# Kernel optimization log

Hardware: AMD Instinct MI355X
Metric: run time of the kernel (lower is better)

The kernel has to match this reference:

```python
import jax, jax.numpy as jnp
import numpy as np

N0, N1, N2 = 80000, 40000, 20000
E1, E2 = 500000, 250000
FIN = 128        # in_channels
H = 2            # heads
C1 = 64          # hidden_channels -> layer1 out per head (concat -> 128)
C2 = 64          # out_channels -> layer2 out per head (mean over heads)
ED = 10          # edge_dim per embedding, total edge feat = 2*ED = 20
NTYPE, NTS = 23, 1158


def setup_inputs() -> dict:
    key = jax.random.key(0)
    ks = jax.random.split(key, 48)
    sc = 0.05
    inp = {
        "x": jax.random.normal(ks[0], (N0, FIN), jnp.float32),
        "ei1_src": jax.random.randint(ks[1], (E1,), 0, N0),
        "ei1_dst": jax.random.randint(ks[2], (E1,), 0, N1),
        "et1": jax.random.randint(ks[3], (E1,), 0, NTYPE),
        "ets1": jax.random.randint(ks[4], (E1,), 0, NTS),
        "ei2_src": jax.random.randint(ks[5], (E2,), 0, N1),
        "ei2_dst": jax.random.randint(ks[6], (E2,), 0, N2),
        "et2": jax.random.randint(ks[7], (E2,), 0, NTYPE),
        "ets2": jax.random.randint(ks[8], (E2,), 0, NTS),
        # shared edge embeddings (Linear(23,10), Linear(1158,10))
        "edge_W": jax.random.normal(ks[9], (ED, NTYPE), jnp.float32) * sc,
        "edge_b": jax.random.normal(ks[10], (ED,), jnp.float32) * sc,
        "time_W": jax.random.normal(ks[11], (ED, NTS), jnp.float32) * sc,
        "time_b": jax.random.normal(ks[12], (ED,), jnp.float32) * sc,
    }
    # layer 1: in=128, heads=2, C=64, concat=True (out dim 128)
    hc1 = H * C1
    inp["Wq1"] = jax.random.normal(ks[13], (hc1, FIN), jnp.float32) * sc
    inp["bq1"] = jnp.zeros((hc1,), jnp.float32)
    inp["Wk1"] = jax.random.normal(ks[14], (hc1, FIN), jnp.float32) * sc
    inp["bk1"] = jnp.zeros((hc1,), jnp.float32)
    inp["Wv1"] = jax.random.normal(ks[15], (hc1, FIN), jnp.float32) * sc
    inp["bv1"] = jnp.zeros((hc1,), jnp.float32)
    inp["We1"] = jax.random.normal(ks[16], (hc1, 2 * ED), jnp.float32) * sc
    inp["Wskip1"] = jax.random.normal(ks[17], (hc1, FIN), jnp.float32) * sc
    inp["bskip1"] = jnp.zeros((hc1,), jnp.float32)
    inp["Wbeta1"] = jax.random.normal(ks[18], (1, 3 * hc1), jnp.float32) * sc
    inp["ln_g"] = jnp.ones((hc1,), jnp.float32)
    inp["ln_b"] = jnp.zeros((hc1,), jnp.float32)
    # layer 2: in=128, heads=2, C=64, concat=False (out dim 64)
    hc2 = H * C2
    inp["Wq2"] = jax.random.normal(ks[19], (hc2, hc1), jnp.float32) * sc
    inp["bq2"] = jnp.zeros((hc2,), jnp.float32)
    inp["Wk2"] = jax.random.normal(ks[20], (hc2, hc1), jnp.float32) * sc
    inp["bk2"] = jnp.zeros((hc2,), jnp.float32)
    inp["Wv2"] = jax.random.normal(ks[21], (hc2, hc1), jnp.float32) * sc
    inp["bv2"] = jnp.zeros((hc2,), jnp.float32)
    inp["We2"] = jax.random.normal(ks[22], (hc2, 2 * ED), jnp.float32) * sc
    inp["Wskip2"] = jax.random.normal(ks[23], (C2, hc1), jnp.float32) * sc
    inp["bskip2"] = jnp.zeros((C2,), jnp.float32)
    inp["Wbeta2"] = jax.random.normal(ks[24], (1, 3 * C2), jnp.float32) * sc
    return inp


def _edge_feat(et, ets, edge_W, edge_b, time_W, time_b):
    # one_hot(e) @ W.T + b == W.T[e] + b (avoids materializing huge one-hot)
    return jnp.concatenate([jnp.take(edge_W.T, et, axis=0) + edge_b,
                            jnp.take(time_W.T, ets, axis=0) + time_b], axis=-1)


def _conv(x_src, x_dst, src, dst, ef, Wq, bq, Wk, bk, Wv, bv, We,
          Wskip, bskip, Wbeta, concat):
    n_dst = x_dst.shape[0]
    HC = Wq.shape[0]
    C = HC // H
    q = (x_dst @ Wq.T + bq).reshape(n_dst, H, C)            # [Nd,H,C]
    k = (x_src @ Wk.T + bk)[src].reshape(-1, H, C)          # [E,H,C]
    v = (x_src @ Wv.T + bv)[src].reshape(-1, H, C)
    e = (ef @ We.T).reshape(-1, H, C)
    k = k + e
    alpha = jnp.einsum('ehc,ehc->eh', q[dst], k) / np.sqrt(C).astype(np.float32)
    # segment softmax over destination nodes
    m = jax.ops.segment_max(alpha, dst, num_segments=n_dst)
    ex = jnp.exp(alpha - m[dst])
    s = jax.ops.segment_sum(ex, dst, num_segments=n_dst)
    a = ex / (s[dst] + 1e-16)                               # [E,H]
    msg = (v + e) * a[..., None]                            # [E,H,C]
    out = jax.ops.segment_sum(msg.reshape(-1, HC), dst, num_segments=n_dst)
    out = out if concat else out.reshape(n_dst, H, C).mean(axis=1)
    x_r = x_dst @ Wskip.T + bskip
    beta = jax.nn.sigmoid(
        jnp.concatenate([out, x_r, out - x_r], axis=-1) @ Wbeta.T)  # [Nd,1]
    return beta * x_r + (1.0 - beta) * out


def _layernorm(x, g, b):
    mu = x.mean(-1, keepdims=True)
    var = x.var(-1, keepdims=True)
    return (x - mu) / jnp.sqrt(var + 1e-5) * g + b


def reference(x, ei1_src, ei1_dst, et1, ets1, ei2_src, ei2_dst, et2, ets2,
              edge_W, edge_b, time_W, time_b,
              Wq1, bq1, Wk1, bk1, Wv1, bv1, We1, Wskip1, bskip1, Wbeta1,
              ln_g, ln_b,
              Wq2, bq2, Wk2, bk2, Wv2, bv2, We2, Wskip2, bskip2, Wbeta2):
    ef1 = _edge_feat(et1, ets1, edge_W, edge_b, time_W, time_b)
    h = _conv(x, x[:N1], ei1_src, ei1_dst, ef1,
              Wq1, bq1, Wk1, bk1, Wv1, bv1, We1, Wskip1, bskip1, Wbeta1,
              concat=True)
    h = jax.nn.gelu(_layernorm(h, ln_g, ln_b), approximate=False)
    ef2 = _edge_feat(et2, ets2, edge_W, edge_b, time_W, time_b)
    o = _conv(h, h[:N2], ei2_src, ei2_dst, ef2,
              Wq2, bq2, Wk2, bk2, Wv2, bv2, We2, Wskip2, bskip2, Wbeta2,
              concat=False)
    return jax.nn.log_softmax(o, axis=-1)
```

## Files before the change

### kernel.cpp

```cpp
#include <hip/hip_runtime.h>
#include <math.h>

#define N0 80000
#define N1 40000
#define N2 20000
#define E1C 500000
#define E2C 250000
#define NTYPE 23
#define NTS 1158

#define NB1 157
#define NB2 79
#define KV1B 1250
#define QR1B 625
#define CNTB 2930
#define KV2B 625
#define QR2B 313
#define FILLB 2930

#define OFF_XB    0u
#define OFF_QR1   5120000u
#define OFF_KV1   15360000u
#define OFF_H     25600000u
#define OFF_QR2   28160000u
#define OFF_KV2   32000000u
#define OFF_WB1   37120000u
#define OFF_BP1   37160000u
#define OFF_WB2   37170000u
#define OFF_BP2   37200000u
#define OFF_TA1   37210000u
#define OFF_TB1   37213000u
#define OFF_TA2   37370000u
#define OFF_TB2   37373000u
#define OFF_RP1   37530000u
#define OFF_CUR1  37580000u
#define OFF_ED1   37630000u
#define OFF_BS1   38640000u
#define OFF_RP2   38650000u
#define OFF_CUR2  38680000u
#define OFF_ED2   38710000u
#define OFF_BS2   39220000u
#define OFF_DONE  39230000u
#define OFF_RK1   39240000u
#define OFF_RK2   39740000u

typedef __bf16 bf16x8 __attribute__((ext_vector_type(8)));
typedef float f32x4 __attribute__((ext_vector_type(4)));

static __device__ __forceinline__ float b2f(unsigned short u) {
    union { unsigned int i; float f; } c;
    c.i = ((unsigned int)u) << 16;
    return c.f;
}
static __device__ __forceinline__ unsigned short f2b(float f) {
    unsigned int u = __float_as_uint(f);
    unsigned int r = (u + 0x7fffu + ((u >> 16) & 1u)) >> 16;
    return (unsigned short)r;
}
static __device__ __forceinline__ bf16x8 ldfrag(const unsigned short* p) {
    return *reinterpret_cast<const bf16x8*>(p);
}

static __device__ __forceinline__ void stage16(const void* g, void* l) {
    __builtin_amdgcn_global_load_lds(
        (const __attribute__((address_space(1))) unsigned int*)g,
        (__attribute__((address_space(3))) unsigned int*)l,
        16, 0, 0);
}

template <int CTRL>
static __device__ __forceinline__ float dpp_addstep(float v) {
    int x = __builtin_amdgcn_mov_dpp(__float_as_int(v), CTRL, 0xF, 0xF, true);
    return v + __int_as_float(x);
}
static __device__ __forceinline__ float red16(float v) {
    v = dpp_addstep<0xB1>(v);
    v = dpp_addstep<0x4E>(v);
    v = dpp_addstep<0x141>(v);
    v = dpp_addstep<0x140>(v);
    return v;
}
template <int CTRL>
static __device__ __forceinline__ float dpp_maxstep(float v) {
    int x = __builtin_amdgcn_mov_dpp(__float_as_int(v), CTRL, 0xF, 0xF, true);
    return fmaxf(v, __int_as_float(x));
}
static __device__ __forceinline__ float red16max(float v) {
    v = dpp_maxstep<0xB1>(v);
    v = dpp_maxstep<0x4E>(v);
    v = dpp_maxstep<0x141>(v);
    v = dpp_maxstep<0x140>(v);
    return v;
}

#define LDSS 136
#define SMEM_USHORTS 16384

template <int NTILES>
static __device__ __forceinline__ void dev_gemm_bf16out(
    const unsigned short* __restrict__ XB, const unsigned short* __restrict__ WB,
    const float* __restrict__ BP, unsigned short* __restrict__ Y, int n, int blk,
    unsigned short* sb) {
    constexpr int COLS = NTILES * 16;
    constexpr int HALF = NTILES / 2;
    constexpr int HCOLS = HALF * 16;
    constexpr int NCHUNK = (NTILES + 3) / 4;
    int wave = threadIdx.x >> 6, lane = threadIdx.x & 63;
    int m = lane & 15, quad = lane >> 4;
    int rowbase = blk * 64 + wave * 16;
    int arow = rowbase + m; if (arow >= n) arow = n - 1;
    unsigned short* swave = sb + wave * 16 * LDSS;
    const unsigned short* xrow = XB + (size_t)arow * 128 + quad * 8;
    bf16x8 a0 = ldfrag(xrow), a1 = ldfrag(xrow + 32);
    bf16x8 a2 = ldfrag(xrow + 64), a3 = ldfrag(xrow + 96);
    f32x4 acc[NTILES];
#pragma unroll
    for (int t = 0; t < NTILES; t++) acc[t] = (f32x4){0.f, 0.f, 0.f, 0.f};
    const char* gstage = (const char*)WB + wave * 1024 + lane * 16;
#pragma unroll
    for (int i = 0; i < 4; i++)
        stage16(gstage + (size_t)i * 4096, (char*)sb + wave * 1024 + i * 4096);
    __syncthreads();
#pragma unroll
    for (int c = 0; c < NCHUNK; c++) {
        if (c + 1 < NCHUNK) {
            char* lbase = (char*)sb + ((c + 1) & 1) * 16384 + wave * 1024;
#pragma unroll
            for (int i = 0; i < 4; i++)
                if ((c + 1) * 4 + i < NTILES)
                    stage16(gstage + (size_t)((c + 1) * 4 + i) * 4096,
                            lbase + i * 4096);
        }
        const unsigned short* cbase = sb + (c & 1) * 8192;
#pragma unroll
        for (int t = 0; t < 4; t++) {
            int tt = c * 4 + t;
            if (tt < NTILES) {
                const unsigned short* wt = cbase + t * 2048 + lane * 8;
                acc[tt] = __builtin_amdgcn_mfma_f32_16x16x32_bf16(a0, ldfrag(wt), acc[tt], 0, 0, 0);
                acc[tt] = __builtin_amdgcn_mfma_f32_16x16x32_bf16(a1, ldfrag(wt + 512), acc[tt], 0, 0, 0);
                acc[tt] = __builtin_amdgcn_mfma_f32_16x16x32_bf16(a2, ldfrag(wt + 1024), acc[tt], 0, 0, 0);
                acc[tt] = __builtin_amdgcn_mfma_f32_16x16x32_bf16(a3, ldfrag(wt + 1536), acc[tt], 0, 0, 0);
            }
        }
        __syncthreads();
    }
    int tswz_bit = (quad >> 1) & 1;
#pragma unroll
    for (int half = 0; half < 2; half++) {
#pragma unroll
        for (int t = 0; t < HALF; t++) {
            int tt = half * HALF + t;
            int tsw = t ^ tswz_bit;
            float b = BP[tt * 16 + m];
#pragma unroll
            for (int r = 0; r < 4; r++)
                swave[(quad * 4 + r) * LDSS + tsw * 16 + m] = f2b(acc[tt][r] + b);
        }
#pragma unroll
        for (int i = 0; i < 4; i++) {
            int idx = i * 64 + lane;
            int r = idx / (HCOLS / 8), g = idx % (HCOLS / 8);
            int gs = g ^ (((r >> 3) & 1) << 1);
            int grow = rowbase + r;
            if (grow < n) {
                uint4 v = *(const uint4*)&swave[r * LDSS + gs * 8];
                *(uint4*)(Y + (size_t)grow * COLS + half * HCOLS + g * 8) = v;
            }
        }
    }
}

template <int NTILES>
static __device__ __forceinline__ void dev_gemm_f32out(
    const unsigned short* __restrict__ XB, const unsigned short* __restrict__ WB,
    const float* __restrict__ BP, float* __restrict__ Y, int n, int blk,
    unsigned short* sb) {
    constexpr int COLS = NTILES * 16;
    constexpr int NCHUNK = (NTILES + 3) / 4;
    int wave = threadIdx.x >> 6, lane = threadIdx.x & 63;
    int m = lane & 15, quad = lane >> 4;
    int rowbase = blk * 64 + wave * 16;
    int arow = rowbase + m; if (arow >= n) arow = n - 1;
    const unsigned short* xrow = XB + (size_t)arow * 128 + quad * 8;
    bf16x8 a0 = ldfrag(xrow), a1 = ldfrag(xrow + 32);
    bf16x8 a2 = ldfrag(xrow + 64), a3 = ldfrag(xrow + 96);
    f32x4 acc[NTILES];
#pragma unroll
    for (int t = 0; t < NTILES; t++) acc[t] = (f32x4){0.f, 0.f, 0.f, 0.f};
    const char* gstage = (const char*)WB + wave * 1024 + lane * 16;
#pragma unroll
    for (int i = 0; i < 4; i++)
        stage16(gstage + (size_t)i * 4096, (char*)sb + wave * 1024 + i * 4096);
    __syncthreads();
#pragma unroll
    for (int c = 0; c < NCHUNK; c++) {
        if (c + 1 < NCHUNK) {
            char* lbase = (char*)sb + ((c + 1) & 1) * 16384 + wave * 1024;
#pragma unroll
            for (int i = 0; i < 4; i++)
                if ((c + 1) * 4 + i < NTILES)
                    stage16(gstage + (size_t)((c + 1) * 4 + i) * 4096,
                            lbase + i * 4096);
        }
        const unsigned short* cbase = sb + (c & 1) * 8192;
#pragma unroll
        for (int t = 0; t < 4; t++) {
            int tt = c * 4 + t;
            if (tt < NTILES) {
                const unsigned short* wt = cbase + t * 2048 + lane * 8;
                acc[tt] = __builtin_amdgcn_mfma_f32_16x16x32_bf16(a0, ldfrag(wt), acc[tt], 0, 0, 0);
                acc[tt] = __builtin_amdgcn_mfma_f32_16x16x32_bf16(a1, ldfrag(wt + 512), acc[tt], 0, 0, 0);
                acc[tt] = __builtin_amdgcn_mfma_f32_16x16x32_bf16(a2, ldfrag(wt + 1024), acc[tt], 0, 0, 0);
                acc[tt] = __builtin_amdgcn_mfma_f32_16x16x32_bf16(a3, ldfrag(wt + 1536), acc[tt], 0, 0, 0);
            }
        }
        __syncthreads();
    }
#pragma unroll
    for (int t = 0; t < NTILES; t++) {
        float b = BP[t * 16 + m];
#pragma unroll
        for (int r = 0; r < 4; r++) {
            int grow = rowbase + quad * 4 + r;
            if (grow < n) Y[(size_t)grow * COLS + t * 16 + m] = acc[t][r] + b;
        }
    }
}

__global__ __launch_bounds__(256) void prep(
    const float* __restrict__ x, unsigned short* __restrict__ XB,
    const float* __restrict__ Wk1, const float* __restrict__ Wv1,
    const float* __restrict__ Wq1, const float* __restrict__ Wskip1,
    const float* __restrict__ bk1, const float* __restrict__ bv1,
    const float* __restrict__ bq1, const float* __restrict__ bskip1,
    const float* __restrict__ Wk2, const float* __restrict__ Wv2,
    const float* __restrict__ Wq2, const float* __restrict__ Wskip2,
    const float* __restrict__ bk2, const float* __restrict__ bv2,
    const float* __restrict__ bq2, const float* __restrict__ bskip2,
    unsigned short* __restrict__ WB1, float* __restrict__ BP1,
    unsigned short* __restrict__ WB2, float* __restrict__ BP2,
    const float* __restrict__ edge_W, const float* __restrict__ edge_b,
    const float* __restrict__ time_W, const float* __restrict__ time_b,
    const float* __restrict__ We1, const float* __restrict__ We2,
    float* __restrict__ TA1, float* __restrict__ TB1,
    float* __restrict__ TA2, float* __restrict__ TB2,
    int* __restrict__ cnt1, int* __restrict__ cnt2, int* __restrict__ done) {
    int tid = blockIdx.x * blockDim.x + threadIdx.x;
    int stride = gridDim.x * blockDim.x;
    for (int i = tid; i < N0 * 32; i += stride) {
        float4 v = *(const float4*)(x + (size_t)i * 4);
        ushort4 u;
        u.x = f2b(v.x); u.y = f2b(v.y); u.z = f2b(v.z); u.w = f2b(v.w);
        *(ushort4*)(XB + (size_t)i * 4) = u;
    }
    for (int i = tid; i < 512 * 128; i += stride) {
        int j = i & 7, l = (i >> 3) & 63, ks = (i >> 9) & 3, t = i >> 11;
        int row = t * 16 + (l & 15);
        int col = ks * 32 + ((l >> 4) & 3) * 8 + j;
        const float* w; int off;
        if (row < 128) { w = Wk1; off = 0; }
        else if (row < 256) { w = Wv1; off = 128; }
        else if (row < 384) { w = Wq1; off = 256; }
        else { w = Wskip1; off = 384; }
        WB1[i] = f2b(w[(size_t)(row - off) * 128 + col]);
    }
    for (int i = tid; i < 512; i += stride) {
        const float* b; int off;
        if (i < 128) { b = bk1; off = 0; }
        else if (i < 256) { b = bv1; off = 128; }
        else if (i < 384) { b = bq1; off = 256; }
        else { b = bskip1; off = 384; }
        BP1[i] = b[i - off];
    }
    for (int i = tid; i < 448 * 128; i += stride) {
        int j = i & 7, l = (i >> 3) & 63, ks = (i >> 9) & 3, t = i >> 11;
        int row = t * 16 + (l & 15);
        int col = ks * 32 + ((l >> 4) & 3) * 8 + j;
        const float* w; int off;
        if (row < 128) { w = Wk2; off = 0; }
        else if (row < 256) { w = Wv2; off = 128; }
        else if (row < 384) { w = Wq2; off = 256; }
        else { w = Wskip2; off = 384; }
        WB2[i] = f2b(w[(size_t)(row - off) * 128 + col]);
    }
    for (int i = tid; i < 448; i += stride) {
        const float* b; int off;
        if (i < 128) { b = bk2; off = 0; }
        else if (i < 256) { b = bv2; off = 128; }
        else if (i < 384) { b = bq2; off = 256; }
        else { b = bskip2; off = 384; }
        BP2[i] = b[i - off];
    }
    const int TBL = (NTYPE + NTS) * 128;
    for (int i = tid; i < TBL; i += stride) {
        if (i < NTYPE * 128) {
            int e = i >> 7, c = i & 127;
            float s1 = 0.f, s2 = 0.f;
#pragma unroll
            for (int j = 0; j < 10; j++) {
                float fj = edge_W[j * NTYPE + e] + edge_b[j];
                s1 += fj * We1[c * 20 + j];
                s2 += fj * We2[c * 20 + j];
            }
            TA1[i] = s1; TA2[i] = s2;
        } else {
            int u = i - NTYPE * 128;
            int ts = u >> 7, c = u & 127;
            float s1 = 0.f, s2 = 0.f;
#pragma unroll
            for (int j = 0; j < 10; j++) {
                float fj = time_W[j * NTS + ts] + time_b[j];
                s1 += fj * We1[c * 20 + 10 + j];
                s2 += fj * We2[c * 20 + 10 + j];
            }
            TB1[u] = s1; TB2[u] = s2;
        }
    }
    for (int i = tid; i < N1 + N2 + 2; i += stride) {
        if (i < N1) cnt1[i] = 0;
        else if (i < N1 + N2) cnt2[i - N1] = 0;
        else done[i - N1 - N2] = 0;
    }
}

__global__ __launch_bounds__(256) void mega_l1(
    const unsigned short* __restrict__ XB,
    const unsigned short* __restrict__ WB1, const float* __restrict__ BP1,
    unsigned short* __restrict__ KV1, float* __restrict__ QR1,
    const int* __restrict__ d1, const int* __restrict__ d2,
    int* __restrict__ cnt1, int* __restrict__ cnt2,
    int* __restrict__ rk1, int* __restrict__ rk2) {
    __shared__ __align__(16) unsigned short sbuf[SMEM_USHORTS];
    int b = blockIdx.x;
    if (b < CNTB) {
        int t = b * 256 + threadIdx.x;
        if (t < E1C) rk1[t] = atomicAdd(&cnt1[d1[t]], 1);
        else {
            t -= E1C;
            if (t < E2C) rk2[t] = atomicAdd(&cnt2[d2[t]], 1);
        }
    } else if (b < CNTB + KV1B) {
        dev_gemm_bf16out<16>(XB, WB1, BP1, KV1, N0, b - CNTB, sbuf);
    } else {
        dev_gemm_f32out<16>(XB, WB1 + 256 * 128, BP1 + 256, QR1, N1,
                            b - CNTB - KV1B, sbuf);
    }
}

__global__ __launch_bounds__(256) void gemm_l2(
    const unsigned short* __restrict__ H,
    const unsigned short* __restrict__ WB2, const float* __restrict__ BP2,
    unsigned short* __restrict__ KV2, float* __restrict__ QR2) {
    __shared__ __align__(16) unsigned short sbuf[SMEM_USHORTS];
    int b = blockIdx.x;
    if (b < KV2B) dev_gemm_bf16out<16>(H, WB2, BP2, KV2, N1, b, sbuf);
    else dev_gemm_f32out<12>(H, WB2 + 256 * 128, BP2 + 256, QR2, N2, b - KV2B, sbuf);
}

__global__ __launch_bounds__(256) void csr_scan(
    int* __restrict__ cnt1, int* __restrict__ bs1, int* __restrict__ rp1,
    int* __restrict__ cnt2, int* __restrict__ bs2, int* __restrict__ rp2,
    int* __restrict__ done) {
    __shared__ int s[256];
    __shared__ int amlast;
    int b = blockIdx.x;
    int* cnt; int* bs; int* rp; int n, lb;
    if (b < NB1) { cnt = cnt1; bs = bs1; rp = rp1; n = N1; lb = b; }
    else { cnt = cnt2; bs = bs2; rp = rp2; n = N2; lb = b - NB1; }
    int t = lb * 256 + threadIdx.x;
    int v = (t < n) ? cnt[t] : 0;
    s[threadIdx.x] = v;
    __syncthreads();
    for (int off = 128; off; off >>= 1) {
        if (threadIdx.x < off) s[threadIdx.x] += s[threadIdx.x + off];
        __syncthreads();
    }
    if (threadIdx.x == 0) {
        atomicExch(&bs[lb], s[0]);
        __threadfence();
        int prev = atomicAdd(&done[0], 1);
        amlast = (prev == NB1 + NB2 - 1) ? 1 : 0;
    }
    __syncthreads();
    if (amlast) {
        int tt = threadIdx.x;
        int v1 = (tt < NB1) ? atomicAdd(&bs1[tt], 0) : 0;
        s[tt] = v1;
        __syncthreads();
        for (int off = 1; off < 256; off <<= 1) {
            int u = (tt >= off) ? s[tt - off] : 0;
            __syncthreads();
            s[tt] += u;
            __syncthreads();
        }
        if (tt < NB1) atomicExch(&bs1[tt], s[tt] - v1);
        __syncthreads();
        int v2 = (tt < NB2) ? atomicAdd(&bs2[tt], 0) : 0;
        s[tt] = v2;
        __syncthreads();
        for (int off = 1; off < 256; off <<= 1) {
            int u = (tt >= off) ? s[tt - off] : 0;
            __syncthreads();
            s[tt] += u;
            __syncthreads();
        }
        if (tt < NB2) atomicExch(&bs2[tt], s[tt] - v2);
        __threadfence();
        __syncthreads();
        if (tt == 0) atomicExch(&done[1], 1);
    }
    if (threadIdx.x == 0) {
        while (atomicAdd(&done[1], 0) == 0) __builtin_amdgcn_s_sleep(1);
    }
    __syncthreads();
    __threadfence();
    int base = atomicAdd(&bs[lb], 0);
    s[threadIdx.x] = v;
    __syncthreads();
    for (int off = 1; off < 256; off <<= 1) {
        int u = (threadIdx.x >= off) ? s[threadIdx.x - off] : 0;
        __syncthreads();
        s[threadIdx.x] += u;
        __syncthreads();
    }
    int incl = s[threadIdx.x];
    if (t < n) rp[t] = base + incl - v;
    if (t == n - 1) rp[n] = base + incl;
}

__global__ __launch_bounds__(256) void fill_both(
    const int* __restrict__ d1, const int* __restrict__ s1,
    const int* __restrict__ et1, const int* __restrict__ ets1,
    const int* __restrict__ rp1, const int* __restrict__ rk1, uint2* __restrict__ ed1,
    const int* __restrict__ d2, const int* __restrict__ s2,
    const int* __restrict__ et2, const int* __restrict__ ets2,
    const int* __restrict__ rp2, const int* __restrict__ rk2, uint2* __restrict__ ed2) {
    int t = blockIdx.x * 256 + threadIdx.x;
    if (t < E1C) {
        int pos = rp1[d1[t]] + rk1[t];
        ed1[pos] = make_uint2((unsigned)s1[t],
                              (unsigned)(et1[t] | (ets1[t] << 16)));
    } else {
        t -= E1C;
        if (t < E2C) {
            int pos = rp2[d2[t]] + rk2[t];
            ed2[pos] = make_uint2((unsigned)s2[t],
                                  (unsigned)(et2[t] | (ets2[t] << 16)));
        }
    }
}

static __device__ __forceinline__ void edge_accum(
    int beg, int end, int s, int co, float4 q4,
    const uint2* __restrict__ ED, const float* __restrict__ TA,
    const float* __restrict__ TB, const unsigned short* __restrict__ KV,
    float& ax, float& ay, float& az, float& aw, float& suma) {
    int p = beg + s;
    if (p >= end) return;

    uint2 dA, dB, dC;
    float4 taA, tbA, taB, tbB, taC, tbC;
    ushort4 kuA, vuA, kuB, vuB, kuC, vuC;

    dA = ED[p];
    int pA = p + 2; bool mA = pA < end;
    dB = ED[mA ? pA : beg];
    int pB = p + 4; bool mB = pB < end;
    dC = ED[mB ? pB : beg];

#define LOADSET(SET, DSC) { \
    int sn_ = (int)DSC.x, t_ = (int)(DSC.y & 0xFFFF), ts_ = (int)(DSC.y >> 16); \
    ta##SET = *(const float4*)(TA + t_ * 128 + co); \
    tb##SET = *(const float4*)(TB + ts_ * 128 + co); \
    const unsigned short* kv_ = KV + (size_t)sn_ * 256; \
    ku##SET = *(const ushort4*)(kv_ + co); \
    vu##SET = *(const ushort4*)(kv_ + 128 + co); }

#define COMPUTE(SET) { \
    float e0c = ta##SET.x + tb##SET.x, e1c = ta##SET.y + tb##SET.y; \
    float e2c = ta##SET.z + tb##SET.z, e3c = ta##SET.w + tb##SET.w; \
    float pp = q4.x * (b2f(ku##SET.x) + e0c) + q4.y * (b2f(ku##SET.y) + e1c) \
             + q4.z * (b2f(ku##SET.z) + e2c) + q4.w * (b2f(ku##SET.w) + e3c); \
    pp = red16(pp); \
    float a = __expf(pp * 0.125f); \
    ax += a * (b2f(vu##SET.x) + e0c); ay += a * (b2f(vu##SET.y) + e1c); \
    az += a * (b2f(vu##SET.z) + e2c); aw += a * (b2f(vu##SET.w) + e3c); \
    suma += a; }

    LOADSET(A, dA)
    LOADSET(B, dB)
    for (;;) {
        {
            int pC = pB + 2; bool mC = pC < end;
            dA = ED[mC ? pC : beg];
            LOADSET(C, dC)
            COMPUTE(A)
            if (!mA) break;
            mA = mB; mB = mC; pB = pC;
        }
        {
            int pC = pB + 2; bool mC = pC < end;
            dB = ED[mC ? pC : beg];
            LOADSET(A, dA)
            COMPUTE(B)
            if (!mA) break;
            mA = mB; mB = mC; pB = pC;
        }
        {
            int pC = pB + 2; bool mC = pC < end;
            dC = ED[mC ? pC : beg];
            LOADSET(B, dB)
            COMPUTE(C)
            if (!mA) break;
            mA = mB; mB = mC; pB = pC;
        }
    }
#undef LOADSET
#undef COMPUTE
}

__global__ __launch_bounds__(256) void agg_layer1(
    const int* __restrict__ rowptr, const uint2* __restrict__ ED,
    const float* __restrict__ TA, const float* __restrict__ TB,
    const float* __restrict__ QR, const unsigned short* __restrict__ KV,
    const float* __restrict__ Wbeta,
    const float* __restrict__ ln_g, const float* __restrict__ ln_b,
    unsigned short* __restrict__ hout, int n) {
    int wid = (blockIdx.x * blockDim.x + threadIdx.x) >> 6;
    int lane = threadIdx.x & 63;
    if (wid >= n) return;
    int s = lane >> 5, cg = lane & 15;
    int co = ((lane >> 4) & 1) * 64 + 4 * cg;
    int beg = rowptr[wid], end = rowptr[wid + 1];
    float4 q4 = *(const float4*)(QR + (size_t)wid * 256 + co);
    float ax = 0.f, ay = 0.f, az = 0.f, aw = 0.f, suma = 0.f;
    edge_accum(beg, end, s, co, q4, ED, TA, TB, KV, ax, ay, az, aw, suma);
    ax += __shfl_xor(ax, 32); ay += __shfl_xor(ay, 32);
    az += __shfl_xor(az, 32); aw += __shfl_xor(aw, 32);
    suma += __shfl_xor(suma, 32);
    float inv_s = 1.f / (suma + 1e-16f);
    float ox = ax * inv_s, oy = ay * inv_s, oz = az * inv_s, ow = aw * inv_s;
    float4 r4 = *(const float4*)(QR + (size_t)wid * 256 + 128 + co);
    float4 wo = *(const float4*)(Wbeta + co);
    float4 wr = *(const float4*)(Wbeta + 128 + co);
    float4 wd = *(const float4*)(Wbeta + 256 + co);
    float pb = wo.x * ox + wr.x * r4.x + wd.x * (ox - r4.x)
             + wo.y * oy + wr.y * r4.y + wd.y * (oy - r4.y)
             + wo.z * oz + wr.z * r4.z + wd.z * (oz - r4.z)
             + wo.w * ow + wr.w * r4.w + wd.w * (ow - r4.w);
    pb = red16(pb);
    pb += __shfl_xor(pb, 16);
    float beta = 1.f / (1.f + __expf(-pb));
    float gx = beta * r4.x + (1.f - beta) * ox;
    float gy = beta * r4.y + (1.f - beta) * oy;
    float gz = beta * r4.z + (1.f - beta) * oz;
    float gw = beta * r4.w + (1.f - beta) * ow;
    float sm = gx + gy + gz + gw;
    float sq = gx * gx + gy * gy + gz * gz + gw * gw;
    sm = red16(sm); sm += __shfl_xor(sm, 16);
    sq = red16(sq); sq += __shfl_xor(sq, 16);
    float mu = sm * (1.f / 128.f);
    float var = sq * (1.f / 128.f) - mu * mu;
    float inv = rsqrtf(var + 1e-5f);
    float4 lg = *(const float4*)(ln_g + co);
    float4 lb = *(const float4*)(ln_b + co);
    float yx = (gx - mu) * inv * lg.x + lb.x;
    float yy = (gy - mu) * inv * lg.y + lb.y;
    float yz = (gz - mu) * inv * lg.z + lb.z;
    float yw = (gw - mu) * inv * lg.w + lb.w;
    const float ISQ2 = 0.70710678118654752f;
    yx = 0.5f * yx * (1.f + erff(yx * ISQ2));
    yy = 0.5f * yy * (1.f + erff(yy * ISQ2));
    yz = 0.5f * yz * (1.f + erff(yz * ISQ2));
    yw = 0.5f * yw * (1.f + erff(yw * ISQ2));
    if (s == 0) {
        ushort4 hv;
        hv.x = f2b(yx); hv.y = f2b(yy); hv.z = f2b(yz); hv.w = f2b(yw);
        *(ushort4*)(hout + (size_t)wid * 128 + co) = hv;
    }
}

__global__ __launch_bounds__(256) void agg_layer2(
    const int* __restrict__ rowptr, const uint2* __restrict__ ED,
    const float* __restrict__ TA, const float* __restrict__ TB,
    const float* __restrict__ QR, const unsigned short* __restrict__ KV,
    const float* __restrict__ Wbeta,
    float* __restrict__ o, int n) {
    int wid = (blockIdx.x * blockDim.x + threadIdx.x) >> 6;
    int lane = threadIdx.x & 63;
    if (wid >= n) return;
    int s = lane >> 5, cg = lane & 15;
    int co = ((lane >> 4) & 1) * 64 + 4 * cg;
    int beg = rowptr[wid], end = rowptr[wid + 1];
    float4 q4 = *(const float4*)(QR + (size_t)wid * 192 + co);
    float ax = 0.f, ay = 0.f, az = 0.f, aw = 0.f, suma = 0.f;
    edge_accum(beg, end, s, co, q4, ED, TA, TB, KV, ax, ay, az, aw, suma);
    ax += __shfl_xor(ax, 32); ay += __shfl_xor(ay, 32);
    az += __shfl_xor(az, 32); aw += __shfl_xor(aw, 32);
    suma += __shfl_xor(suma, 32);
    float inv_s = 1.f / (suma + 1e-16f);
    float ox = ax * inv_s, oy = ay * inv_s, oz = az * inv_s, ow = aw * inv_s;
    ox = 0.5f * (ox + __shfl_xor(ox, 16));
    oy = 0.5f * (oy + __shfl_xor(oy, 16));
    oz = 0.5f * (oz + __shfl_xor(oz, 16));
    ow = 0.5f * (ow + __shfl_xor(ow, 16));
    float4 r4 = *(const float4*)(QR + (size_t)wid * 192 + 128 + 4 * cg);
    float4 wo = *(const float4*)(Wbeta + 4 * cg);
    float4 wr = *(const float4*)(Wbeta + 64 + 4 * cg);
    float4 wd = *(const float4*)(Wbeta + 128 + 4 * cg);
    float pb = wo.x * ox + wr.x * r4.x + wd.x * (ox - r4.x)
             + wo.y * oy + wr.y * r4.y + wd.y * (oy - r4.y)
             + wo.z * oz + wr.z * r4.z + wd.z * (oz - r4.z)
             + wo.w * ow + wr.w * r4.w + wd.w * (ow - r4.w);
    pb = red16(pb);
    float beta = 1.f / (1.f + __expf(-pb));
    float vx = beta * r4.x + (1.f - beta) * ox;
    float vy = beta * r4.y + (1.f - beta) * oy;
    float vz = beta * r4.z + (1.f - beta) * oz;
    float vw = beta * r4.w + (1.f - beta) * ow;
    float m = fmaxf(fmaxf(vx, vy), fmaxf(vz, vw));
    m = red16max(m);
    float se = __expf(vx - m) + __expf(vy - m) + __expf(vz - m) + __expf(vw - m);
    se = red16(se);
    float lse = m + logf(se);
    if (lane < 16)
        *(float4*)(o + (size_t)wid * 64 + 4 * cg) =
            make_float4(vx - lse, vy - lse, vz - lse, vw - lse);
}

extern "C" void kernel_launch(void* const* d_in, const int* in_sizes, int n_in,
                              void* d_out, int out_size, void* d_ws, size_t ws_size,
                              hipStream_t stream) {
    const float* x        = (const float*)d_in[0];
    const int*   ei1_src  = (const int*)d_in[1];
    const int*   ei1_dst  = (const int*)d_in[2];
    const int*   et1      = (const int*)d_in[3];
    const int*   ets1     = (const int*)d_in[4];
    const int*   ei2_src  = (const int*)d_in[5];
    const int*   ei2_dst  = (const int*)d_in[6];
    const int*   et2      = (const int*)d_in[7];
    const int*   ets2     = (const int*)d_in[8];
    const float* edge_W   = (const float*)d_in[9];
    const float* edge_b   = (const float*)d_in[10];
    const float* time_W   = (const float*)d_in[11];
    const float* time_b   = (const float*)d_in[12];
    const float* Wq1      = (const float*)d_in[13];
    const float* bq1      = (const float*)d_in[14];
    const float* Wk1      = (const float*)d_in[15];
    const float* bk1      = (const float*)d_in[16];
    const float* Wv1      = (const float*)d_in[17];
    const float* bv1      = (const float*)d_in[18];
    const float* We1      = (const float*)d_in[19];
    const float* Wskip1   = (const float*)d_in[20];
    const float* bskip1   = (const float*)d_in[21];
    const float* Wbeta1   = (const float*)d_in[22];
    const float* ln_g     = (const float*)d_in[23];
    const float* ln_b     = (const float*)d_in[24];
    const float* Wq2      = (const float*)d_in[25];
    const float* bq2      = (const float*)d_in[26];
    const float* Wk2      = (const float*)d_in[27];
    const float* bk2      = (const float*)d_in[28];
    const float* Wv2      = (const float*)d_in[29];
    const float* bv2      = (const float*)d_in[30];
    const float* We2      = (const float*)d_in[31];
    const float* Wskip2   = (const float*)d_in[32];
    const float* bskip2   = (const float*)d_in[33];
    const float* Wbeta2   = (const float*)d_in[34];

    float* ws = (float*)d_ws;
    unsigned short* xb  = (unsigned short*)(ws + OFF_XB);
    float* qr1          = ws + OFF_QR1;
    unsigned short* kv1 = (unsigned short*)(ws + OFF_KV1);
    unsigned short* h   = (unsigned short*)(ws + OFF_H);
    float* qr2          = ws + OFF_QR2;
    unsigned short* kv2 = (unsigned short*)(ws + OFF_KV2);
    unsigned short* wb1 = (unsigned short*)(ws + OFF_WB1);
    float* bp1          = ws + OFF_BP1;
    unsigned short* wb2 = (unsigned short*)(ws + OFF_WB2);
    float* bp2          = ws + OFF_BP2;
    float* ta1          = ws + OFF_TA1;
    float* tb1          = ws + OFF_TB1;
    float* ta2          = ws + OFF_TA2;
    float* tb2          = ws + OFF_TB2;
    int*   rp1          = (int*)(ws + OFF_RP1);
    int*   cur1         = (int*)(ws + OFF_CUR1);
    uint2* ed1          = (uint2*)(ws + OFF_ED1);
    int*   bs1          = (int*)(ws + OFF_BS1);
    int*   rp2          = (int*)(ws + OFF_RP2);
    int*   cur2         = (int*)(ws + OFF_CUR2);
    uint2* ed2          = (uint2*)(ws + OFF_ED2);
    int*   bs2          = (int*)(ws + OFF_BS2);
    int*   done         = (int*)(ws + OFF_DONE);
    int*   rk1          = (int*)(ws + OFF_RK1);
    int*   rk2          = (int*)(ws + OFF_RK2);

    prep<<<2048, 256, 0, stream>>>(
        x, xb,
        Wk1, Wv1, Wq1, Wskip1, bk1, bv1, bq1, bskip1,
        Wk2, Wv2, Wq2, Wskip2, bk2, bv2, bq2, bskip2,
        wb1, bp1, wb2, bp2,
        edge_W, edge_b, time_W, time_b, We1, We2,
        ta1, tb1, ta2, tb2, cur1, cur2, done);
    mega_l1<<<KV1B + QR1B + CNTB, 256, 0, stream>>>(
        xb, wb1, bp1, kv1, qr1, ei1_dst, ei2_dst, cur1, cur2, rk1, rk2);
    csr_scan<<<NB1 + NB2, 256, 0, stream>>>(cur1, bs1, rp1, cur2, bs2, rp2, done);
    fill_both<<<FILLB, 256, 0, stream>>>(
        ei1_dst, ei1_src, et1, ets1, rp1, rk1, ed1,
        ei2_dst, ei2_src, et2, ets2, rp2, rk2, ed2);
    agg_layer1<<<(N1 + 3) / 4, 256, 0, stream>>>(rp1, ed1,
        ta1, tb1, qr1, kv1, Wbeta1, ln_g, ln_b, h, N1);
    gemm_l2<<<KV2B + QR2B, 256, 0, stream>>>(h, wb2, bp2, kv2, qr2);
    agg_layer2<<<(N2 + 3) / 4, 256, 0, stream>>>(rp2, ed2,
        ta2, tb2, qr2, kv2, Wbeta2, (float*)d_out, N2);
}
```

Baseline: 354.5 us.

## Precompute combined bf16 edge-embedding table for all type/timestamp pairs

```diff
diff --git a/kernel.cpp b/kernel.cpp
--- a/kernel.cpp
+++ b/kernel.cpp
@@ -17,8 +17,12 @@
 #define KV2B 625
 #define QR2B 313
 #define FILLB 2930
+#define TCB  1800
+#define NTC  (NTYPE * NTS)
 
 #define OFF_XB    0u
+#define OFF_TC1   0u
+#define OFF_TC2   1710000u
 #define OFF_QR1   5120000u
 #define OFF_KV1   15360000u
 #define OFF_H     25600000u
@@ -46,11 +50,18 @@
 
 typedef __bf16 bf16x8 __attribute__((ext_vector_type(8)));
 typedef float f32x4 __attribute__((ext_vector_type(4)));
+typedef float f32x2 __attribute__((ext_vector_type(2)));
 
 static __device__ __forceinline__ float b2f(unsigned short u) {
     union { unsigned int i; float f; } c;
     c.i = ((unsigned int)u) << 16;
     return c.f;
+}
+static __device__ __forceinline__ f32x2 b2f2(unsigned int u) {
+    f32x2 r;
+    r.x = __uint_as_float(u << 16);
+    r.y = __uint_as_float(u & 0xFFFF0000u);
+    return r;
 }
 static __device__ __forceinline__ unsigned short f2b(float f) {
     unsigned int u = __float_as_uint(f);
@@ -361,10 +372,35 @@
 __global__ __launch_bounds__(256) void csr_scan(
     int* __restrict__ cnt1, int* __restrict__ bs1, int* __restrict__ rp1,
     int* __restrict__ cnt2, int* __restrict__ bs2, int* __restrict__ rp2,
-    int* __restrict__ done) {
+    int* __restrict__ done,
+    const float* __restrict__ TA1, const float* __restrict__ TB1,
+    const float* __restrict__ TA2, const float* __restrict__ TB2,
+    unsigned short* __restrict__ TC1, unsigned short* __restrict__ TC2) {
+    int b = blockIdx.x;
+    if (b >= NB1 + NB2) {
+        const int UNITS = NTC * 16;
+        int bid = b - (NB1 + NB2);
+        for (int i = bid * 256 + threadIdx.x; i < 2 * UNITS; i += TCB * 256) {
+            int tab = (i >= UNITS);
+            int j = tab ? i - UNITS : i;
+            int tidx = j >> 4, c8 = (j & 15) << 3;
+            int t = tidx / NTS, ts = tidx - t * NTS;
+            const float* ta = (tab ? TA2 : TA1) + t * 128 + c8;
+            const float* tb = (tab ? TB2 : TB1) + ts * 128 + c8;
+            unsigned short* o = (tab ? TC2 : TC1) + (size_t)tidx * 128 + c8;
+            float4 a0 = *(const float4*)ta, a1 = *(const float4*)(ta + 4);
+            float4 b0 = *(const float4*)tb, b1 = *(const float4*)(tb + 4);
+            ushort4 o0, o1;
+            o0.x = f2b(a0.x + b0.x); o0.y = f2b(a0.y + b0.y);
+            o0.z = f2b(a0.z + b0.z); o0.w = f2b(a0.w + b0.w);
+            o1.x = f2b(a1.x + b1.x); o1.y = f2b(a1.y + b1.y);
+            o1.z = f2b(a1.z + b1.z); o1.w = f2b(a1.w + b1.w);
+            *(ushort4*)o = o0; *(ushort4*)(o + 4) = o1;
+        }
+        return;
+    }
     __shared__ int s[256];
     __shared__ int amlast;
-    int b = blockIdx.x;
     int* cnt; int* bs; int* rp; int n, lb;
     if (b < NB1) { cnt = cnt1; bs = bs1; rp = rp1; n = N1; lb = b; }
     else { cnt = cnt2; bs = bs2; rp = rp2; n = N2; lb = b - NB1; }
@@ -440,89 +476,65 @@
     if (t < E1C) {
         int pos = rp1[d1[t]] + rk1[t];
         ed1[pos] = make_uint2((unsigned)s1[t],
-                              (unsigned)(et1[t] | (ets1[t] << 16)));
+                              (unsigned)((et1[t] * NTS + ets1[t]) * 128));
     } else {
         t -= E1C;
         if (t < E2C) {
             int pos = rp2[d2[t]] + rk2[t];
             ed2[pos] = make_uint2((unsigned)s2[t],
-                                  (unsigned)(et2[t] | (ets2[t] << 16)));
+                                  (unsigned)((et2[t] * NTS + ets2[t]) * 128));
         }
     }
 }
 
 static __device__ __forceinline__ void edge_accum(
-    int beg, int end, int s, int co, float4 q4,
-    const uint2* __restrict__ ED, const float* __restrict__ TA,
-    const float* __restrict__ TB, const unsigned short* __restrict__ KV,
-    float& ax, float& ay, float& az, float& aw, float& suma) {
+    int beg, int end, int s, int co, f32x2 q01, f32x2 q23,
+    const uint2* __restrict__ ED, const unsigned short* __restrict__ TCl,
+    const unsigned short* __restrict__ KV,
+    f32x2& acc01, f32x2& acc23, float& suma) {
     int p = beg + s;
     if (p >= end) return;
-
-    uint2 dA, dB, dC;
-    float4 taA, tbA, taB, tbB, taC, tbC;
-    ushort4 kuA, vuA, kuB, vuB, kuC, vuC;
-
-    dA = ED[p];
-    int pA = p + 2; bool mA = pA < end;
-    dB = ED[mA ? pA : beg];
-    int pB = p + 4; bool mB = pB < end;
-    dC = ED[mB ? pB : beg];
-
-#define LOADSET(SET, DSC) { \
-    int sn_ = (int)DSC.x, t_ = (int)(DSC.y & 0xFFFF), ts_ = (int)(DSC.y >> 16); \
-    ta##SET = *(const float4*)(TA + t_ * 128 + co); \
-    tb##SET = *(const float4*)(TB + ts_ * 128 + co); \
-    const unsigned short* kv_ = KV + (size_t)sn_ * 256; \
-    ku##SET = *(const ushort4*)(kv_ + co); \
-    vu##SET = *(const ushort4*)(kv_ + 128 + co); }
-
-#define COMPUTE(SET) { \
-    float e0c = ta##SET.x + tb##SET.x, e1c = ta##SET.y + tb##SET.y; \
-    float e2c = ta##SET.z + tb##SET.z, e3c = ta##SET.w + tb##SET.w; \
-    float pp = q4.x * (b2f(ku##SET.x) + e0c) + q4.y * (b2f(ku##SET.y) + e1c) \
-             + q4.z * (b2f(ku##SET.z) + e2c) + q4.w * (b2f(ku##SET.w) + e3c); \
-    pp = red16(pp); \
-    float a = __expf(pp * 0.125f); \
-    ax += a * (b2f(vu##SET.x) + e0c); ay += a * (b2f(vu##SET.y) + e1c); \
-    az += a * (b2f(vu##SET.z) + e2c); aw += a * (b2f(vu##SET.w) + e3c); \
-    suma += a; }
-
-    LOADSET(A, dA)
-    LOADSET(B, dB)
+    uint2 d0 = ED[p];
+    int pA = p + 2;  bool mA = pA < end;
+    uint2 d1 = ED[mA ? pA : beg];
+    int pB = p + 4;  bool mB = pB < end;
+    uint2 d2 = ED[mB ? pB : beg];
+    uint2 tc0 = *(const uint2*)(TCl + d0.y);
+    const unsigned short* kv0 = KV + (size_t)d0.x * 256;
+    uint2 ku0 = *(const uint2*)(kv0 + co);
+    uint2 vu0 = *(const uint2*)(kv0 + 128 + co);
+    uint2 tc1 = *(const uint2*)(TCl + d1.y);
+    const unsigned short* kv1 = KV + (size_t)d1.x * 256;
+    uint2 ku1 = *(const uint2*)(kv1 + co);
+    uint2 vu1 = *(const uint2*)(kv1 + 128 + co);
     for (;;) {
-        {
-            int pC = pB + 2; bool mC = pC < end;
-            dA = ED[mC ? pC : beg];
-            LOADSET(C, dC)
-            COMPUTE(A)
-            if (!mA) break;
-            mA = mB; mB = mC; pB = pC;
-        }
-        {
-            int pC = pB + 2; bool mC = pC < end;
-            dB = ED[mC ? pC : beg];
-            LOADSET(A, dA)
-            COMPUTE(B)
-            if (!mA) break;
-            mA = mB; mB = mC; pB = pC;
-        }
-        {
-            int pC = pB + 2; bool mC = pC < end;
-            dC = ED[mC ? pC : beg];
-            LOADSET(B, dB)
-            COMPUTE(C)
-            if (!mA) break;
-            mA = mB; mB = mC; pB = pC;
-        }
-    }
-#undef LOADSET
-#undef COMPUTE
+        int pC = pB + 2; bool mC = pC < end;
+        uint2 d3 = ED[mC ? pC : beg];
+        uint2 tc2 = *(const uint2*)(TCl + d2.y);
+        const unsigned short* kv2 = KV + (size_t)d2.x * 256;
+        uint2 ku2 = *(const uint2*)(kv2 + co);
+        uint2 vu2 = *(const uint2*)(kv2 + 128 + co);
+        f32x2 e01 = b2f2(tc0.x), e23 = b2f2(tc0.y);
+        f32x2 k01 = b2f2(ku0.x) + e01, k23 = b2f2(ku0.y) + e23;
+        f32x2 pp2 = q01 * k01 + q23 * k23;
+        float pp = pp2.x + pp2.y;
+        pp = red16(pp);
+        float a = __expf(pp * 0.125f);
+        f32x2 v01 = b2f2(vu0.x) + e01, v23 = b2f2(vu0.y) + e23;
+        f32x2 av = {a, a};
+        acc01 += av * v01; acc23 += av * v23;
+        suma += a;
+        if (!mA) break;
+        tc0 = tc1; ku0 = ku1; vu0 = vu1;
+        tc1 = tc2; ku1 = ku2; vu1 = vu2;
+        d2 = d3;
+        mA = mB; mB = mC; pB = pC;
+    }
 }
 
 __global__ __launch_bounds__(256) void agg_layer1(
     const int* __restrict__ rowptr, const uint2* __restrict__ ED,
-    const float* __restrict__ TA, const float* __restrict__ TB,
+    const unsigned short* __restrict__ TC,
     const float* __restrict__ QR, const unsigned short* __restrict__ KV,
     const float* __restrict__ Wbeta,
     const float* __restrict__ ln_g, const float* __restrict__ ln_b,
@@ -534,8 +546,11 @@
     int co = ((lane >> 4) & 1) * 64 + 4 * cg;
     int beg = rowptr[wid], end = rowptr[wid + 1];
     float4 q4 = *(const float4*)(QR + (size_t)wid * 256 + co);
-    float ax = 0.f, ay = 0.f, az = 0.f, aw = 0.f, suma = 0.f;
-    edge_accum(beg, end, s, co, q4, ED, TA, TB, KV, ax, ay, az, aw, suma);
+    f32x2 q01 = {q4.x, q4.y}, q23 = {q4.z, q4.w};
+    f32x2 acc01 = {0.f, 0.f}, acc23 = {0.f, 0.f};
+    float suma = 0.f;
+    edge_accum(beg, end, s, co, q01, q23, ED, TC + co, KV, acc01, acc23, suma);
+    float ax = acc01.x, ay = acc01.y, az = acc23.x, aw = acc23.y;
     ax += __shfl_xor(ax, 32); ay += __shfl_xor(ay, 32);
     az += __shfl_xor(az, 32); aw += __shfl_xor(aw, 32);
     suma += __shfl_xor(suma, 32);
@@ -583,7 +598,7 @@
 
 __global__ __launch_bounds__(256) void agg_layer2(
     const int* __restrict__ rowptr, const uint2* __restrict__ ED,
-    const float* __restrict__ TA, const float* __restrict__ TB,
+    const unsigned short* __restrict__ TC,
     const float* __restrict__ QR, const unsigned short* __restrict__ KV,
     const float* __restrict__ Wbeta,
     float* __restrict__ o, int n) {
@@ -594,8 +609,11 @@
     int co = ((lane >> 4) & 1) * 64 + 4 * cg;
     int beg = rowptr[wid], end = rowptr[wid + 1];
     float4 q4 = *(const float4*)(QR + (size_t)wid * 192 + co);
-    float ax = 0.f, ay = 0.f, az = 0.f, aw = 0.f, suma = 0.f;
-    edge_accum(beg, end, s, co, q4, ED, TA, TB, KV, ax, ay, az, aw, suma);
+    f32x2 q01 = {q4.x, q4.y}, q23 = {q4.z, q4.w};
+    f32x2 acc01 = {0.f, 0.f}, acc23 = {0.f, 0.f};
+    float suma = 0.f;
+    edge_accum(beg, end, s, co, q01, q23, ED, TC + co, KV, acc01, acc23, suma);
+    float ax = acc01.x, ay = acc01.y, az = acc23.x, aw = acc23.y;
     ax += __shfl_xor(ax, 32); ay += __shfl_xor(ay, 32);
     az += __shfl_xor(az, 32); aw += __shfl_xor(aw, 32);
     suma += __shfl_xor(suma, 32);
@@ -670,6 +688,8 @@
 
     float* ws = (float*)d_ws;
     unsigned short* xb  = (unsigned short*)(ws + OFF_XB);
+    unsigned short* tc1 = (unsigned short*)(ws + OFF_TC1);
+    unsigned short* tc2 = (unsigned short*)(ws + OFF_TC2);
     float* qr1          = ws + OFF_QR1;
     unsigned short* kv1 = (unsigned short*)(ws + OFF_KV1);
     unsigned short* h   = (unsigned short*)(ws + OFF_H);
@@ -704,13 +724,15 @@
         ta1, tb1, ta2, tb2, cur1, cur2, done);
     mega_l1<<<KV1B + QR1B + CNTB, 256, 0, stream>>>(
         xb, wb1, bp1, kv1, qr1, ei1_dst, ei2_dst, cur1, cur2, rk1, rk2);
-    csr_scan<<<NB1 + NB2, 256, 0, stream>>>(cur1, bs1, rp1, cur2, bs2, rp2, done);
+    csr_scan<<<NB1 + NB2 + TCB, 256, 0, stream>>>(
+        cur1, bs1, rp1, cur2, bs2, rp2, done,
+        ta1, tb1, ta2, tb2, tc1, tc2);
     fill_both<<<FILLB, 256, 0, stream>>>(
         ei1_dst, ei1_src, et1, ets1, rp1, rk1, ed1,
         ei2_dst, ei2_src, et2, ets2, rp2, rk2, ed2);
     agg_layer1<<<(N1 + 3) / 4, 256, 0, stream>>>(rp1, ed1,
-        ta1, tb1, qr1, kv1, Wbeta1, ln_g, ln_b, h, N1);
+        tc1, qr1, kv1, Wbeta1, ln_g, ln_b, h, N1);
     gemm_l2<<<KV2B + QR2B, 256, 0, stream>>>(h, wb2, bp2, kv2, qr2);
     agg_layer2<<<(N2 + 3) / 4, 256, 0, stream>>>(rp2, ed2,
-        ta2, tb2, qr2, kv2, Wbeta2, (float*)d_out, N2);
-}
+        tc2, qr2, kv2, Wbeta2, (float*)d_out, N2);
+}
```

Result: slower. 373.7 us (+5.4%).
